# Kernel tuning notes

Measured on AMD Instinct MI355X. Metric: run time of the kernel, lower is better.

## Reference

```python
import jax, jax.numpy as jnp
import numpy as np

NEG_SLOPE = 0.2
LN_EPS = 1e-5
NUM_LAYERS = 4
H = 3            # num heads (both modalities)
C_MOL = 512      # molecule channels (in == out, required by the cat in forward)
C_PROT = 1280    # protein channels
VOCAB = 512 * 9 + 1
G_MOL = 512      # molecule graphs
G_PROT = 32      # protein graphs


def _with_self_loops(src, dst, n):
    loop = jnp.arange(n, dtype=src.dtype)
    return jnp.concatenate([src, loop]), jnp.concatenate([dst, loop])


def gat_conv(x, src, dst, W, a_src, a_dst, bias):
    """PyG GATConv, concat=False (head-mean), add_self_loops=True.
    x: [N, Fin], W: [Fin, H*C], a_src/a_dst: [H, C], bias: [C]."""
    n = x.shape[0]
    h = (x @ W).reshape(n, a_src.shape[0], a_src.shape[1])   # [N,H,C]
    al_s = jnp.sum(h * a_src, axis=-1)                       # [N,H]
    al_d = jnp.sum(h * a_dst, axis=-1)                       # [N,H]
    s, d = _with_self_loops(src, dst, n)
    e = jax.nn.leaky_relu(al_s[s] + al_d[d], NEG_SLOPE)      # [E+N,H]
    m = jax.ops.segment_max(e, d, num_segments=n)            # segment softmax (stable)
    m = jnp.where(jnp.isfinite(m), m, 0.0)
    p = jnp.exp(e - m[d])
    z = jax.ops.segment_sum(p, d, num_segments=n)
    alpha = p / (z[d] + 1e-16)                               # [E+N,H]
    out = jax.ops.segment_sum(h[s] * alpha[:, :, None], d, num_segments=n)  # [N,H,C]
    return out.mean(axis=1) + bias                           # concat=False -> head mean


def layer_norm(x, g, b):
    mu = x.mean(-1, keepdims=True)
    var = ((x - mu) ** 2).mean(-1, keepdims=True)
    return (x - mu) * jax.lax.rsqrt(var + LN_EPS) * g + b


def mean_pool(x, batch, num_graphs):
    s = jax.ops.segment_sum(x, batch, num_segments=num_graphs)
    cnt = jax.ops.segment_sum(jnp.ones((x.shape[0],), x.dtype), batch, num_segments=num_graphs)
    return s / jnp.maximum(cnt, 1.0)[:, None]


def setup_inputs() -> dict:
    key = jax.random.key(0)
    ks = jax.random.split(key, 20)
    n_mol, e_mol = 40000, 80000
    n_prot, e_prot = 8000, 64000
    drug_x = jax.random.randint(ks[0], (n_mol, 9), 0, VOCAB)
    mol_edge_index = jax.random.randint(ks[1], (2, e_mol), 0, n_mol)
    mol_batch = jnp.sort(jax.random.randint(ks[2], (n_mol,), 0, G_MOL))
    prot_x = jax.random.normal(ks[3], (n_prot, C_PROT), jnp.float32)
    prot_edge_index = jax.random.randint(ks[4], (2, e_prot), 0, n_prot)
    prot_batch = jnp.sort(jax.random.randint(ks[5], (n_prot,), 0, G_PROT))
    sc = 0.02
    emb = (jax.random.normal(ks[6], (VOCAB, C_MOL), jnp.float32) * sc).at[0].set(0.0)  # padding_idx=0
    mol_W = jax.random.normal(ks[7], (NUM_LAYERS, C_MOL, H * C_MOL), jnp.float32) * sc
    mol_asrc = jax.random.normal(ks[8], (NUM_LAYERS, H, C_MOL), jnp.float32) * sc
    mol_adst = jax.random.normal(ks[9], (NUM_LAYERS, H, C_MOL), jnp.float32) * sc
    mol_bias = jnp.zeros((NUM_LAYERS, C_MOL), jnp.float32)
    mol_ln_g = jnp.ones((NUM_LAYERS, C_MOL), jnp.float32)
    mol_ln_b = jnp.zeros((NUM_LAYERS, C_MOL), jnp.float32)
    prot_W = jax.random.normal(ks[10], (NUM_LAYERS, C_PROT, H * C_PROT), jnp.float32) * sc
    prot_asrc = jax.random.normal(ks[11], (NUM_LAYERS, H, C_PROT), jnp.float32) * sc
    prot_adst = jax.random.normal(ks[12], (NUM_LAYERS, H, C_PROT), jnp.float32) * sc
    prot_bias = jnp.zeros((NUM_LAYERS, C_PROT), jnp.float32)
    prot_ln_g = jnp.ones((NUM_LAYERS, C_PROT), jnp.float32)
    prot_ln_b = jnp.zeros((NUM_LAYERS, C_PROT), jnp.float32)
    return dict(drug_x=drug_x, mol_edge_index=mol_edge_index, mol_batch=mol_batch,
                prot_x=prot_x, prot_edge_index=prot_edge_index, prot_batch=prot_batch,
                emb=emb, mol_W=mol_W, mol_asrc=mol_asrc, mol_adst=mol_adst,
                mol_bias=mol_bias, mol_ln_g=mol_ln_g, mol_ln_b=mol_ln_b,
                prot_W=prot_W, prot_asrc=prot_asrc, prot_adst=prot_adst,
                prot_bias=prot_bias, prot_ln_g=prot_ln_g, prot_ln_b=prot_ln_b)


def reference(drug_x, mol_edge_index, mol_batch, prot_x, prot_edge_index, prot_batch,
              emb, mol_W, mol_asrc, mol_adst, mol_bias, mol_ln_g, mol_ln_b,
              prot_W, prot_asrc, prot_adst, prot_bias, prot_ln_g, prot_ln_b):
    # dropout layers are identity (eval mode)
    mol_x = emb[drug_x].mean(axis=-2)                       # [N_mol, C_MOL]
    mol_feats = [mean_pool(mol_x, mol_batch, G_MOL)]
    prot_feats = [mean_pool(prot_x, prot_batch, G_PROT)]
    msrc, mdst = mol_edge_index[0], mol_edge_index[1]
    psrc, pdst = prot_edge_index[0], prot_edge_index[1]
    px = prot_x
    for i in range(NUM_LAYERS):
        mol_x = gat_conv(mol_x, msrc, mdst, mol_W[i], mol_asrc[i], mol_adst[i], mol_bias[i])
        mol_x = layer_norm(mol_x, mol_ln_g[i], mol_ln_b[i])
        px = gat_conv(px, psrc, pdst, prot_W[i], prot_asrc[i], prot_adst[i], prot_bias[i])
        px = layer_norm(px, prot_ln_g[i], prot_ln_b[i])
        mol_feats.append(mean_pool(mol_x, mol_batch, G_MOL))
        prot_feats.append(mean_pool(px, prot_batch, G_PROT))
    return jnp.stack(mol_feats, axis=1), jnp.stack(prot_feats, axis=1)  # [G,5,C] each
```

## Files before the change

### kernel.cpp

```cpp
#include <hip/hip_runtime.h>
#include <cstdint>


constexpr int H_HEADS = 3;
constexpr float NEG_SLOPE = 0.2f;
constexpr float LN_EPS = 1e-5f;
constexpr int N_MOL = 40000, E_MOL = 80000, C_MOL = 512, G_MOL = 512;
constexpr int N_PROT = 8000, E_PROT = 64000, C_PROT = 1280, G_PROT = 32;
constexpr int LAYERS = 4;
constexpr int MPAD_MOL = 40064;
constexpr int MPAD_PROT = 8064;

typedef unsigned short u16;
typedef __attribute__((ext_vector_type(8))) short short8v;
typedef __attribute__((ext_vector_type(4))) unsigned short ushort4v;
typedef __attribute__((ext_vector_type(4))) float f32x4;

__device__ __forceinline__ float bf2f(u16 s) {
    union { unsigned u; float f; } v; v.u = ((unsigned)s) << 16; return v.f;
}
__device__ __forceinline__ u16 f2bf(float f) {
    union { float f; unsigned u; } v; v.f = f;
    return (u16)((v.u + 0x7fffu + ((v.u >> 16) & 1u)) >> 16);
}

__device__ __forceinline__ void g2l16(const void* g, void* l) {
    __builtin_amdgcn_global_load_lds((const __attribute__((address_space(1))) void*)g,
                                     (__attribute__((address_space(3))) void*)l, 16, 0, 0);
}


__global__ void set_int_kernel(int* p, int v, int n) {
    int i = blockIdx.x * blockDim.x + threadIdx.x;
    if (i < n) p[i] = v;
}

__global__ void zero_f32_kernel(float* p, int n) {
    int i = blockIdx.x * blockDim.x + threadIdx.x;
    if (i < n) p[i] = 0.f;
}

__global__ void copy_int_kernel(const int* __restrict__ s, int* __restrict__ d, int n) {
    int i = blockIdx.x * blockDim.x + threadIdx.x;
    if (i < n) d[i] = s[i];
}

__global__ void hist_kernel(const int* __restrict__ keys, int n, int* __restrict__ cnt) {
    int i = blockIdx.x * blockDim.x + threadIdx.x;
    if (i < n) atomicAdd(&cnt[keys[i]], 1);
}

__global__ void scan_kernel(const int* __restrict__ in, int* __restrict__ out, int n) {
    __shared__ int sums[1024];
    const int t = threadIdx.x;
    const int chunk = (n + 1023) / 1024;
    const int start = t * chunk;
    const int end = min(start + chunk, n);
    int s = 0;
    for (int i = start; i < end; ++i) s += in[i];
    sums[t] = s;
    __syncthreads();
    if (t == 0) {
        int acc = 0;
        for (int i = 0; i < 1024; ++i) { int v = sums[i]; sums[i] = acc; acc += v; }
        out[n] = acc;
    }
    __syncthreads();
    int acc = sums[t];
    for (int i = start; i < end; ++i) { out[i] = acc; acc += in[i]; }
}

__global__ void fill_self_kernel(int* __restrict__ pos, int* __restrict__ srcl, int n) {
    int i = blockIdx.x * blockDim.x + threadIdx.x;
    if (i < n) { int slot = atomicAdd(&pos[i], 1); srcl[slot] = i; }
}

__global__ void fill_edge_kernel(const int* __restrict__ src, const int* __restrict__ dst, int e,
                                 int* __restrict__ pos, int* __restrict__ srcl) {
    int i = blockIdx.x * blockDim.x + threadIdx.x;
    if (i < e) { int slot = atomicAdd(&pos[dst[i]], 1); srcl[slot] = src[i]; }
}

__global__ void f32_to_bf16(const float* __restrict__ in, u16* __restrict__ out, int n) {
    int i = blockIdx.x * blockDim.x + threadIdx.x;
    if (i < n) out[i] = f2bf(in[i]);
}


__global__ void embed_mean_kernel(const int* __restrict__ drug_x, const float* __restrict__ emb,
                                  u16* __restrict__ out) {
    const int n = blockIdx.x;
    __shared__ int idx[9];
    if (threadIdx.x < 9) idx[threadIdx.x] = drug_x[n * 9 + threadIdx.x];
    __syncthreads();
    const int c = threadIdx.x;
    float s = 0.f;
#pragma unroll
    for (int t = 0; t < 9; ++t) s += emb[(size_t)idx[t] * C_MOL + c];
    out[(size_t)n * C_MOL + c] = f2bf(s * (1.f / 9.f));
}


template <int CIN, int COUT>
__global__ __launch_bounds__(256) void fold_attn(const float* __restrict__ W,
                                                 const float* __restrict__ asrc,
                                                 const float* __restrict__ adst,
                                                 float* __restrict__ wsrc, float* __restrict__ wdst) {
    const int i = blockIdx.x;
    const int tid = threadIdx.x;
    __shared__ float rb[8];
    const float* Wr = W + (size_t)i * (H_HEADS * COUT);
    for (int h = 0; h < H_HEADS; ++h) {
        float ss = 0.f, sd = 0.f;
        for (int c = tid; c < COUT; c += 256) {
            const float w = Wr[h * COUT + c];
            ss += w * asrc[h * COUT + c];
            sd += w * adst[h * COUT + c];
        }
        for (int o = 32; o; o >>= 1) { ss += __shfl_down(ss, o); sd += __shfl_down(sd, o); }
        if ((tid & 63) == 0) { rb[tid >> 6] = ss; rb[4 + (tid >> 6)] = sd; }
        __syncthreads();
        if (tid == 0) {
            wsrc[h * CIN + i] = rb[0] + rb[1] + rb[2] + rb[3];
            wdst[h * CIN + i] = rb[4] + rb[5] + rb[6] + rb[7];
        }
        __syncthreads();
    }
}


__global__ __launch_bounds__(256) void transposeW(const float* __restrict__ W, u16* __restrict__ Wt,
                                                  int COUT, size_t headStride, int ldn) {
    __shared__ float t[32][33];
    const int h = blockIdx.z;
    const int n0 = blockIdx.x * 32, k0 = blockIdx.y * 32;
    const int tx = threadIdx.x & 31, ty = threadIdx.x >> 5;
#pragma unroll
    for (int q = 0; q < 4; ++q)
        t[ty + q * 8][tx] = W[(size_t)(k0 + ty + q * 8) * (H_HEADS * COUT) + h * COUT + n0 + tx];
    __syncthreads();
#pragma unroll
    for (int q = 0; q < 4; ++q)
        Wt[(size_t)h * headStride + (size_t)(n0 + ty + q * 8) * ldn + k0 + tx] =
            f2bf(t[tx][ty + q * 8]);
}


template <int C>
__global__ void attn_logits(const u16* __restrict__ x, const float* __restrict__ wsrc,
                            const float* __restrict__ wdst, float* __restrict__ als,
                            float* __restrict__ ald) {
    constexpr int PER = C / 64;
    const int n = blockIdx.x, lane = threadIdx.x;
    const u16* xr = x + (size_t)n * C + lane * PER;
    float xv[PER];
#pragma unroll
    for (int i = 0; i < PER; i += 4) {
        const ushort4v v = *(const ushort4v*)(xr + i);
        xv[i] = bf2f(v.x); xv[i + 1] = bf2f(v.y); xv[i + 2] = bf2f(v.z); xv[i + 3] = bf2f(v.w);
    }
    for (int h = 0; h < H_HEADS; ++h) {
        const float* ws = wsrc + h * C + lane * PER;
        const float* wd = wdst + h * C + lane * PER;
        float ss = 0.f, sd = 0.f;
#pragma unroll
        for (int i = 0; i < PER; i += 4) {
            const float4 a = *(const float4*)(ws + i);
            const float4 b = *(const float4*)(wd + i);
            ss += xv[i] * a.x + xv[i + 1] * a.y + xv[i + 2] * a.z + xv[i + 3] * a.w;
            sd += xv[i] * b.x + xv[i + 1] * b.y + xv[i + 2] * b.z + xv[i + 3] * b.w;
        }
        for (int o = 32; o; o >>= 1) { ss += __shfl_down(ss, o); sd += __shfl_down(sd, o); }
        if (lane == 0) { als[n * H_HEADS + h] = ss; ald[n * H_HEADS + h] = sd; }
    }
}


__global__ void alpha_kernel(const float* __restrict__ als, const float* __restrict__ ald,
                             const int* __restrict__ indptr, const int* __restrict__ srcl,
                             float* __restrict__ alphaw) {
    const int n = blockIdx.x, lane = threadIdx.x;
    if (lane >= H_HEADS) return;
    const int beg = indptr[n], end = indptr[n + 1];
    const float ad = ald[n * H_HEADS + lane];
    float m = -1e30f;
    for (int e = beg; e < end; ++e) {
        float v = als[srcl[e] * H_HEADS + lane] + ad;
        v = v >= 0.f ? v : NEG_SLOPE * v;
        m = fmaxf(m, v);
    }
    float z = 0.f;
    for (int e = beg; e < end; ++e) {
        float v = als[srcl[e] * H_HEADS + lane] + ad;
        v = v >= 0.f ? v : NEG_SLOPE * v;
        z += __expf(v - m);
    }
    const float zi = 1.f / (z + 1e-16f);
    for (int e = beg; e < end; ++e) {
        float v = als[srcl[e] * H_HEADS + lane] + ad;
        v = v >= 0.f ? v : NEG_SLOPE * v;
        alphaw[e * H_HEADS + lane] = __expf(v - m) * zi;
    }
}


template <int C>
__global__ void aggregate_head(const u16* __restrict__ x, const float* __restrict__ alphaw,
                               const int* __restrict__ indptr, const int* __restrict__ srcl,
                               int head, u16* __restrict__ aggH) {
    const int n = blockIdx.x, tid = threadIdx.x;
    const int beg = indptr[n], end = indptr[n + 1];
    float a0 = 0.f, a1 = 0.f, a2 = 0.f, a3 = 0.f;
    for (int e = beg; e < end; ++e) {
        const float a = alphaw[e * H_HEADS + head];
        const ushort4v v = *(const ushort4v*)(x + (size_t)srcl[e] * C + tid * 4);
        a0 += a * bf2f(v.x); a1 += a * bf2f(v.y); a2 += a * bf2f(v.z); a3 += a * bf2f(v.w);
    }
    ushort4v r;
    r.x = f2bf(a0); r.y = f2bf(a1); r.z = f2bf(a2); r.w = f2bf(a3);
    *(ushort4v*)(aggH + (size_t)n * C + tid * 4) = r;
}


template <int C>
__global__ void aggregate_all3(const u16* __restrict__ x, const float* __restrict__ alphaw,
                               const int* __restrict__ indptr, const int* __restrict__ srcl,
                               u16* __restrict__ aggAll) {
    const int n = blockIdx.x, tid = threadIdx.x;
    const int beg = indptr[n], end = indptr[n + 1];
    float acc[H_HEADS][4];
#pragma unroll
    for (int h = 0; h < H_HEADS; ++h)
#pragma unroll
        for (int j = 0; j < 4; ++j) acc[h][j] = 0.f;
    for (int e = beg; e < end; ++e) {
        const float a0 = alphaw[e * H_HEADS + 0];
        const float a1 = alphaw[e * H_HEADS + 1];
        const float a2 = alphaw[e * H_HEADS + 2];
        const ushort4v v = *(const ushort4v*)(x + (size_t)srcl[e] * C + tid * 4);
        const float f0 = bf2f(v.x), f1 = bf2f(v.y), f2 = bf2f(v.z), f3 = bf2f(v.w);
        acc[0][0] += a0 * f0; acc[0][1] += a0 * f1; acc[0][2] += a0 * f2; acc[0][3] += a0 * f3;
        acc[1][0] += a1 * f0; acc[1][1] += a1 * f1; acc[1][2] += a1 * f2; acc[1][3] += a1 * f3;
        acc[2][0] += a2 * f0; acc[2][1] += a2 * f1; acc[2][2] += a2 * f2; acc[2][3] += a2 * f3;
    }
    u16* o = aggAll + (size_t)n * (3 * C) + tid * 4;
#pragma unroll
    for (int h = 0; h < H_HEADS; ++h) {
        ushort4v r;
        r.x = f2bf(acc[h][0]); r.y = f2bf(acc[h][1]); r.z = f2bf(acc[h][2]); r.w = f2bf(acc[h][3]);
        *(ushort4v*)(o + h * C) = r;
    }
}


template <int BETA>
__global__ __launch_bounds__(256) void gemm_mfma(const u16* __restrict__ A,
                                                 const u16* __restrict__ Bt,
                                                 u16* __restrict__ C, int M, int N, int K) {
    __shared__ u16 As[64][40];
    __shared__ u16 Bs[256][40];
    const int tid = threadIdx.x;
    const int w = tid >> 6;
    const int l = tid & 63;
    const int bm = blockIdx.y * 64;
    const int bn = blockIdx.x * 256;
    const f32x4 zf = {0.f, 0.f, 0.f, 0.f};
    f32x4 acc[4][4];
#pragma unroll
    for (int i = 0; i < 4; ++i)
#pragma unroll
        for (int j = 0; j < 4; ++j) acc[i][j] = zf;

    const int arow = tid >> 2, aseg = tid & 3;
    const u16* Ab = A + (size_t)(bm + arow) * K + aseg * 8;
    for (int k0 = 0; k0 < K; k0 += 32) {
        const float4 av = *(const float4*)(Ab + k0);
        float4 bv[4];
#pragma unroll
        for (int q = 0; q < 4; ++q) {
            const int c = q * 256 + tid;
            bv[q] = *(const float4*)(Bt + (size_t)(bn + (c >> 2)) * K + k0 + (c & 3) * 8);
        }
        __syncthreads();
        *(float4*)&As[arow][aseg * 8] = av;
#pragma unroll
        for (int q = 0; q < 4; ++q) {
            const int c = q * 256 + tid;
            *(float4*)&Bs[c >> 2][(c & 3) * 8] = bv[q];
        }
        __syncthreads();
        const int koff = 8 * (l >> 4);
        const int rl = l & 15;
        short8v af[4], bfr[4];
#pragma unroll
        for (int fm = 0; fm < 4; ++fm) af[fm] = *(const short8v*)&As[fm * 16 + rl][koff];
#pragma unroll
        for (int fn = 0; fn < 4; ++fn) bfr[fn] = *(const short8v*)&Bs[w * 64 + fn * 16 + rl][koff];
#pragma unroll
        for (int fm = 0; fm < 4; ++fm)
#pragma unroll
            for (int fn = 0; fn < 4; ++fn)
                acc[fm][fn] =
                    __builtin_amdgcn_mfma_f32_16x16x32_bf16(af[fm], bfr[fn], acc[fm][fn], 0, 0, 0);
    }
    const int r0 = (l >> 4) * 4;
    const int cn = l & 15;
#pragma unroll
    for (int fm = 0; fm < 4; ++fm)
#pragma unroll
        for (int fn = 0; fn < 4; ++fn) {
            u16* Cp = C + (size_t)(bm + fm * 16 + r0) * N + bn + w * 64 + fn * 16 + cn;
#pragma unroll
            for (int r = 0; r < 4; ++r) {
                float v = acc[fm][fn][r];
                if (BETA) v += bf2f(Cp[(size_t)r * N]);
                Cp[(size_t)r * N] = f2bf(v);
            }
        }
}


__global__ __launch_bounds__(256) void gemm_mfma128(const u16* __restrict__ A,
                                                    const u16* __restrict__ Bt,
                                                    u16* __restrict__ Cout,
                                                    int M, int N, int K) {
    __shared__ u16 lds[17408];
    const int tid = threadIdx.x;
    const int w = tid >> 6, l = tid & 63;
    const int wr = w >> 1, wc = w & 1;
    const size_t bm = (size_t)blockIdx.y * 128, bn = (size_t)blockIdx.x * 128;
    const f32x4 zf = {0.f, 0.f, 0.f, 0.f};
    f32x4 acc[4][4];
#pragma unroll
    for (int i = 0; i < 4; ++i)
#pragma unroll
        for (int j = 0; j < 4; ++j) acc[i][j] = zf;

    const int srow = w * 32 + (l >> 3);
    const int sseg = (l & 7) ^ (l >> 3);
    const u16* Ab = A + (bm + srow) * (size_t)K + sseg * 8;
    const u16* Bb = Bt + (bn + srow) * (size_t)K + sseg * 8;

    for (int k0 = 0; k0 < K; k0 += 64) {
#pragma unroll
        for (int q = 0; q < 4; ++q)
            g2l16(Ab + k0 + (size_t)q * 8 * K, lds + (w * 4 + q) * 512);
#pragma unroll
        for (int q = 0; q < 4; ++q)
            g2l16(Bb + k0 + (size_t)q * 8 * K, lds + 8192 + (w * 4 + q) * 512);
        __syncthreads();
#pragma unroll
        for (int kk = 0; kk < 2; ++kk) {
            short8v af[4], bfr[4];
#pragma unroll
            for (int fm = 0; fm < 4; ++fm) {
                const int row = wr * 64 + fm * 16 + (l & 15);
                const int seg = (kk * 4 + (l >> 4)) ^ (row & 7);
                af[fm] = *(const short8v*)&lds[row * 64 + seg * 8];
            }
#pragma unroll
            for (int fn = 0; fn < 4; ++fn) {
                const int row = wc * 64 + fn * 16 + (l & 15);
                const int seg = (kk * 4 + (l >> 4)) ^ (row & 7);
                bfr[fn] = *(const short8v*)&lds[8192 + row * 64 + seg * 8];
            }
#pragma unroll
            for (int fm = 0; fm < 4; ++fm)
#pragma unroll
                for (int fn = 0; fn < 4; ++fn)
                    acc[fm][fn] = __builtin_amdgcn_mfma_f32_16x16x32_bf16(af[fm], bfr[fn],
                                                                          acc[fm][fn], 0, 0, 0);
        }
        __syncthreads();
    }

#pragma unroll
    for (int fm = 0; fm < 4; ++fm) {
        const int row = wr * 64 + fm * 16 + (l >> 4) * 4;
#pragma unroll
        for (int fn = 0; fn < 4; ++fn) {
            const int col = wc * 64 + fn * 16 + (l & 15);
#pragma unroll
            for (int r = 0; r < 4; ++r) lds[(row + r) * 136 + col] = f2bf(acc[fm][fn][r]);
        }
    }
    __syncthreads();
    const int orow = tid >> 1, ohalf = tid & 1;
    u16* Crow = Cout + (bm + orow) * (size_t)N + bn + ohalf * 64;
    const u16* Lrow = lds + orow * 136 + ohalf * 64;
#pragma unroll
    for (int i = 0; i < 8; ++i)
        *(float4*)(Crow + i * 8) = *(const float4*)(Lrow + i * 8);
}


template <int C>
__global__ __launch_bounds__(256) void ln_kernel(const u16* __restrict__ acc,
                                                 const float* __restrict__ bias,
                                                 const float* __restrict__ g,
                                                 const float* __restrict__ b,
                                                 u16* __restrict__ xout) {
    constexpr int PER = C / 256;
    const int n = blockIdx.x, tid = threadIdx.x;
    const u16* ar = acc + (size_t)n * C;
    float vals[PER];
    float s1 = 0.f, s2 = 0.f;
    constexpr float invH = 1.f / (float)H_HEADS;
#pragma unroll
    for (int i = 0; i < PER; ++i) {
        const int c = i * 256 + tid;
        const float v = bf2f(ar[c]) * invH + bias[c];
        vals[i] = v;
        s1 += v;
        s2 += v * v;
    }
    __shared__ float red[2][4];
    for (int o = 32; o; o >>= 1) { s1 += __shfl_down(s1, o); s2 += __shfl_down(s2, o); }
    if ((tid & 63) == 0) { red[0][tid >> 6] = s1; red[1][tid >> 6] = s2; }
    __syncthreads();
    const float t1 = red[0][0] + red[0][1] + red[0][2] + red[0][3];
    const float t2 = red[1][0] + red[1][1] + red[1][2] + red[1][3];
    const float mu = t1 / C;
    const float var = t2 / C - mu * mu;
    const float rstd = rsqrtf(var + LN_EPS);
    u16* xr = xout + (size_t)n * C;
#pragma unroll
    for (int i = 0; i < PER; ++i) {
        const int c = i * 256 + tid;
        xr[c] = f2bf((vals[i] - mu) * rstd * g[c] + b[c]);
    }
}


template <int C, int S>
__global__ void pool_atomic(const u16* __restrict__ x, const int* __restrict__ goff,
                            float* __restrict__ out, int layer) {
    const int g = blockIdx.x, seg = blockIdx.y;
    const int beg = goff[g], end = goff[g + 1];
    const int len = end - beg;
    const int s0 = beg + (len * seg) / S;
    const int s1 = beg + (len * (seg + 1)) / S;
    if (s0 >= s1) return;
    const float inv = 1.f / fmaxf((float)len, 1.f);
    const int tid = threadIdx.x;
    float a0 = 0.f, a1 = 0.f, a2 = 0.f, a3 = 0.f;
    for (int n = s0; n < s1; ++n) {
        const ushort4v v = *(const ushort4v*)(x + (size_t)n * C + tid * 4);
        a0 += bf2f(v.x); a1 += bf2f(v.y); a2 += bf2f(v.z); a3 += bf2f(v.w);
    }
    float* o = out + ((size_t)g * (LAYERS + 1) + layer) * C + tid * 4;
    atomicAdd(o + 0, a0 * inv);
    atomicAdd(o + 1, a1 * inv);
    atomicAdd(o + 2, a2 * inv);
    atomicAdd(o + 3, a3 * inv);
}


extern "C" void kernel_launch(void* const* d_in, const int* in_sizes, int n_in, void* d_out,
                              int out_size, void* d_ws, size_t ws_size, hipStream_t stream) {
    const int* drug_x      = (const int*)d_in[0];
    const int* mol_ei      = (const int*)d_in[1];
    const int* mol_batch   = (const int*)d_in[2];
    const float* prot_in   = (const float*)d_in[3];
    const int* prot_ei     = (const int*)d_in[4];
    const int* prot_batch  = (const int*)d_in[5];
    const float* emb       = (const float*)d_in[6];
    const float* mol_W     = (const float*)d_in[7];
    const float* mol_asrc  = (const float*)d_in[8];
    const float* mol_adst  = (const float*)d_in[9];
    const float* mol_bias  = (const float*)d_in[10];
    const float* mol_lng   = (const float*)d_in[11];
    const float* mol_lnb   = (const float*)d_in[12];
    const float* prot_W    = (const float*)d_in[13];
    const float* prot_asrc = (const float*)d_in[14];
    const float* prot_adst = (const float*)d_in[15];
    const float* prot_bias = (const float*)d_in[16];
    const float* prot_lng  = (const float*)d_in[17];
    const float* prot_lnb  = (const float*)d_in[18];

    if (ws_size < (size_t)157000000) return;
    const bool BIG = ws_size >= (size_t)240500000;

    char* base = (char*)d_ws;
    size_t off = 0;
    auto alloc = [&](size_t bytes) -> void* {
        void* r = base + off;
        off = (off + bytes + 255) & ~(size_t)255;
        return r;
    };
    u16* x_mol  = (u16*)alloc((size_t)N_MOL * C_MOL * 2);
    u16* x_prot = (u16*)alloc((size_t)N_PROT * C_PROT * 2);
    u16* Wt     = (u16*)alloc((size_t)H_HEADS * C_PROT * C_PROT * 2);
    float* wsrc = (float*)alloc((size_t)H_HEADS * C_PROT * 4);
    float* wdst = (float*)alloc((size_t)H_HEADS * C_PROT * 4);
    float* als  = (float*)alloc((size_t)N_MOL * H_HEADS * 4);
    float* ald  = (float*)alloc((size_t)N_MOL * H_HEADS * 4);
    float* alphaw = (float*)alloc((size_t)(E_MOL + N_MOL) * H_HEADS * 4);
    int* mol_indptr  = (int*)alloc((N_MOL + 1) * 4);
    int* mol_pos     = (int*)alloc(N_MOL * 4);
    int* mol_srcl    = (int*)alloc((E_MOL + N_MOL) * 4);
    int* prot_indptr = (int*)alloc((N_PROT + 1) * 4);
    int* prot_pos    = (int*)alloc(N_PROT * 4);
    int* prot_srcl   = (int*)alloc((E_PROT + N_PROT) * 4);
    int* cnt         = (int*)alloc(N_MOL * 4);
    int* mol_goff    = (int*)alloc((G_MOL + 1) * 4);
    int* prot_goff   = (int*)alloc((G_PROT + 1) * 4);
    int* gcnt        = (int*)alloc(G_MOL * 4);
    u16 *aggAll = nullptr, *aggH = nullptr, *outb = nullptr;
    if (BIG) {
        aggAll = (u16*)alloc((size_t)3 * MPAD_MOL * C_MOL * 2);
        outb   = (u16*)alloc((size_t)MPAD_MOL * C_MOL * 2);
    } else {
        aggH = (u16*)alloc((size_t)N_MOL * C_MOL * 2);
        outb = (u16*)alloc((size_t)N_MOL * C_MOL * 2);
    }

    float* out_mol  = (float*)d_out;
    float* out_prot = (float*)d_out + (size_t)G_MOL * (LAYERS + 1) * C_MOL;

    zero_f32_kernel<<<(out_size + 255) / 256, 256, 0, stream>>>((float*)d_out, out_size);

    set_int_kernel<<<(N_MOL + 255) / 256, 256, 0, stream>>>(cnt, 1, N_MOL);
    hist_kernel<<<(E_MOL + 255) / 256, 256, 0, stream>>>(mol_ei + E_MOL, E_MOL, cnt);
    scan_kernel<<<1, 1024, 0, stream>>>(cnt, mol_indptr, N_MOL);
    copy_int_kernel<<<(N_MOL + 255) / 256, 256, 0, stream>>>(mol_indptr, mol_pos, N_MOL);
    fill_self_kernel<<<(N_MOL + 255) / 256, 256, 0, stream>>>(mol_pos, mol_srcl, N_MOL);
    fill_edge_kernel<<<(E_MOL + 255) / 256, 256, 0, stream>>>(mol_ei, mol_ei + E_MOL, E_MOL, mol_pos,
                                                              mol_srcl);

    set_int_kernel<<<(N_PROT + 255) / 256, 256, 0, stream>>>(cnt, 1, N_PROT);
    hist_kernel<<<(E_PROT + 255) / 256, 256, 0, stream>>>(prot_ei + E_PROT, E_PROT, cnt);
    scan_kernel<<<1, 1024, 0, stream>>>(cnt, prot_indptr, N_PROT);
    copy_int_kernel<<<(N_PROT + 255) / 256, 256, 0, stream>>>(prot_indptr, prot_pos, N_PROT);
    fill_self_kernel<<<(N_PROT + 255) / 256, 256, 0, stream>>>(prot_pos, prot_srcl, N_PROT);
    fill_edge_kernel<<<(E_PROT + 255) / 256, 256, 0, stream>>>(prot_ei, prot_ei + E_PROT, E_PROT,
                                                               prot_pos, prot_srcl);

    set_int_kernel<<<(G_MOL + 255) / 256, 256, 0, stream>>>(gcnt, 0, G_MOL);
    hist_kernel<<<(N_MOL + 255) / 256, 256, 0, stream>>>(mol_batch, N_MOL, gcnt);
    scan_kernel<<<1, 1024, 0, stream>>>(gcnt, mol_goff, G_MOL);
    set_int_kernel<<<(G_PROT + 255) / 256, 256, 0, stream>>>(gcnt, 0, G_PROT);
    hist_kernel<<<(N_PROT + 255) / 256, 256, 0, stream>>>(prot_batch, N_PROT, gcnt);
    scan_kernel<<<1, 1024, 0, stream>>>(gcnt, prot_goff, G_PROT);

    f32_to_bf16<<<(N_PROT * C_PROT + 255) / 256, 256, 0, stream>>>(prot_in, x_prot, N_PROT * C_PROT);
    embed_mean_kernel<<<N_MOL, C_MOL, 0, stream>>>(drug_x, emb, x_mol);
    pool_atomic<C_MOL, 8><<<dim3(G_MOL, 8), C_MOL / 4, 0, stream>>>(x_mol, mol_goff, out_mol, 0);
    pool_atomic<C_PROT, 64><<<dim3(G_PROT, 64), C_PROT / 4, 0, stream>>>(x_prot, prot_goff, out_prot, 0);

    for (int l = 0; l < LAYERS; ++l) {
        {
            const float* Wl = mol_W + (size_t)l * C_MOL * (H_HEADS * C_MOL);
            fold_attn<C_MOL, C_MOL><<<C_MOL, 256, 0, stream>>>(
                Wl, mol_asrc + (size_t)l * H_HEADS * C_MOL, mol_adst + (size_t)l * H_HEADS * C_MOL,
                wsrc, wdst);
            attn_logits<C_MOL><<<N_MOL, 64, 0, stream>>>(x_mol, wsrc, wdst, als, ald);
            alpha_kernel<<<N_MOL, 64, 0, stream>>>(als, ald, mol_indptr, mol_srcl, alphaw);
            if (BIG) {
                transposeW<<<dim3(C_MOL / 32, C_MOL / 32, H_HEADS), 256, 0, stream>>>(
                    Wl, Wt, C_MOL, (size_t)C_MOL, 3 * C_MOL);
                aggregate_all3<C_MOL><<<N_MOL, C_MOL / 4, 0, stream>>>(x_mol, alphaw, mol_indptr,
                                                                       mol_srcl, aggAll);
                gemm_mfma128<<<dim3(C_MOL / 128, MPAD_MOL / 128), 256, 0, stream>>>(
                    aggAll, Wt, outb, MPAD_MOL, C_MOL, 3 * C_MOL);
            } else {
                transposeW<<<dim3(C_MOL / 32, C_MOL / 32, H_HEADS), 256, 0, stream>>>(
                    Wl, Wt, C_MOL, (size_t)C_MOL * C_MOL, C_MOL);
                for (int h = 0; h < H_HEADS; ++h) {
                    aggregate_head<C_MOL><<<N_MOL, C_MOL / 4, 0, stream>>>(x_mol, alphaw, mol_indptr,
                                                                           mol_srcl, h, aggH);
                    const u16* Bh = Wt + (size_t)h * C_MOL * C_MOL;
                    if (h == 0)
                        gemm_mfma<0><<<dim3(C_MOL / 256, N_MOL / 64), 256, 0, stream>>>(
                            aggH, Bh, outb, N_MOL, C_MOL, C_MOL);
                    else
                        gemm_mfma<1><<<dim3(C_MOL / 256, N_MOL / 64), 256, 0, stream>>>(
                            aggH, Bh, outb, N_MOL, C_MOL, C_MOL);
                }
            }
            ln_kernel<C_MOL><<<N_MOL, 256, 0, stream>>>(outb, mol_bias + (size_t)l * C_MOL,
                                                        mol_lng + (size_t)l * C_MOL,
                                                        mol_lnb + (size_t)l * C_MOL, x_mol);
            pool_atomic<C_MOL, 8><<<dim3(G_MOL, 8), C_MOL / 4, 0, stream>>>(x_mol, mol_goff, out_mol,
                                                                            l + 1);
        }
        {
            const float* Wl = prot_W + (size_t)l * C_PROT * (H_HEADS * C_PROT);
            fold_attn<C_PROT, C_PROT><<<C_PROT, 256, 0, stream>>>(
                Wl, prot_asrc + (size_t)l * H_HEADS * C_PROT,
                prot_adst + (size_t)l * H_HEADS * C_PROT, wsrc, wdst);
            attn_logits<C_PROT><<<N_PROT, 64, 0, stream>>>(x_prot, wsrc, wdst, als, ald);
            alpha_kernel<<<N_PROT, 64, 0, stream>>>(als, ald, prot_indptr, prot_srcl, alphaw);
            if (BIG) {
                transposeW<<<dim3(C_PROT / 32, C_PROT / 32, H_HEADS), 256, 0, stream>>>(
                    Wl, Wt, C_PROT, (size_t)C_PROT, 3 * C_PROT);
                aggregate_all3<C_PROT><<<N_PROT, C_PROT / 4, 0, stream>>>(x_prot, alphaw, prot_indptr,
                                                                          prot_srcl, aggAll);
                gemm_mfma128<<<dim3(C_PROT / 128, MPAD_PROT / 128), 256, 0, stream>>>(
                    aggAll, Wt, outb, MPAD_PROT, C_PROT, 3 * C_PROT);
            } else {
                transposeW<<<dim3(C_PROT / 32, C_PROT / 32, H_HEADS), 256, 0, stream>>>(
                    Wl, Wt, C_PROT, (size_t)C_PROT * C_PROT, C_PROT);
                for (int h = 0; h < H_HEADS; ++h) {
                    aggregate_head<C_PROT><<<N_PROT, C_PROT / 4, 0, stream>>>(
                        x_prot, alphaw, prot_indptr, prot_srcl, h, aggH);
                    const u16* Bh = Wt + (size_t)h * C_PROT * C_PROT;
                    if (h == 0)
                        gemm_mfma<0><<<dim3(C_PROT / 256, N_PROT / 64), 256, 0, stream>>>(
                            aggH, Bh, outb, N_PROT, C_PROT, C_PROT);
                    else
                        gemm_mfma<1><<<dim3(C_PROT / 256, N_PROT / 64), 256, 0, stream>>>(
                            aggH, Bh, outb, N_PROT, C_PROT, C_PROT);
                }
            }
            ln_kernel<C_PROT><<<N_PROT, 256, 0, stream>>>(outb, prot_bias + (size_t)l * C_PROT,
                                                          prot_lng + (size_t)l * C_PROT,
                                                          prot_lnb + (size_t)l * C_PROT, x_prot);
            pool_atomic<C_PROT, 64><<<dim3(G_PROT, 64), C_PROT / 4, 0, stream>>>(x_prot, prot_goff,
                                                                                 out_prot, l + 1);
        }
    }
}
```

Baseline: 2.372 ms.

## Fuse attention logits into LayerNorm, add 256-wide XCD-swizzled GEMM, wave-per-node aggregation

Several changes land together. Attention-vector folding is hoisted for all layers up front, and the next layer's per-node attention logits are computed inside the LayerNorm kernel, which removes one pass over the activations per layer. The softmax-weight kernel now uses one thread per (node, head) instead of a mostly idle 64-thread block per node. Molecule aggregation processes one node per wave with 8-wide loads. A new 128x256-tile GEMM with 512 threads and XCD-aware block remapping replaces the 128x128 GEMM, and the small-workspace fallback path is removed. The larger GEMM tile raises LDS use and register pressure, and the logit fusion adds reductions to the LayerNorm kernel.

```diff
diff --git a/kernel.cpp b/kernel.cpp
--- a/kernel.cpp
+++ b/kernel.cpp
@@ -176,49 +176,67 @@
 }
 
 
-__global__ void alpha_kernel(const float* __restrict__ als, const float* __restrict__ ald,
-                             const int* __restrict__ indptr, const int* __restrict__ srcl,
-                             float* __restrict__ alphaw) {
-    const int n = blockIdx.x, lane = threadIdx.x;
-    if (lane >= H_HEADS) return;
+__global__ void alpha_kernel2(const float* __restrict__ als, const float* __restrict__ ald,
+                              const int* __restrict__ indptr, const int* __restrict__ srcl,
+                              float* __restrict__ alphaw, int n_nodes) {
+    const int t = blockIdx.x * blockDim.x + threadIdx.x;
+    const int n = t / H_HEADS, h = t - n * H_HEADS;
+    if (n >= n_nodes) return;
     const int beg = indptr[n], end = indptr[n + 1];
-    const float ad = ald[n * H_HEADS + lane];
+    const float ad = ald[n * H_HEADS + h];
     float m = -1e30f;
     for (int e = beg; e < end; ++e) {
-        float v = als[srcl[e] * H_HEADS + lane] + ad;
+        float v = als[srcl[e] * H_HEADS + h] + ad;
         v = v >= 0.f ? v : NEG_SLOPE * v;
         m = fmaxf(m, v);
     }
     float z = 0.f;
     for (int e = beg; e < end; ++e) {
-        float v = als[srcl[e] * H_HEADS + lane] + ad;
+        float v = als[srcl[e] * H_HEADS + h] + ad;
         v = v >= 0.f ? v : NEG_SLOPE * v;
         z += __expf(v - m);
     }
     const float zi = 1.f / (z + 1e-16f);
     for (int e = beg; e < end; ++e) {
-        float v = als[srcl[e] * H_HEADS + lane] + ad;
+        float v = als[srcl[e] * H_HEADS + h] + ad;
         v = v >= 0.f ? v : NEG_SLOPE * v;
-        alphaw[e * H_HEADS + lane] = __expf(v - m) * zi;
-    }
-}
-
-
-template <int C>
-__global__ void aggregate_head(const u16* __restrict__ x, const float* __restrict__ alphaw,
-                               const int* __restrict__ indptr, const int* __restrict__ srcl,
-                               int head, u16* __restrict__ aggH) {
-    const int n = blockIdx.x, tid = threadIdx.x;
+        alphaw[e * H_HEADS + h] = __expf(v - m) * zi;
+    }
+}
+
+
+__global__ __launch_bounds__(256) void aggregate_mol(const u16* __restrict__ x,
+                                                     const float* __restrict__ alphaw,
+                                                     const int* __restrict__ indptr,
+                                                     const int* __restrict__ srcl,
+                                                     u16* __restrict__ aggAll) {
+    const int wv = threadIdx.x >> 6, lane = threadIdx.x & 63;
+    const int n = blockIdx.x * 4 + wv;
     const int beg = indptr[n], end = indptr[n + 1];
-    float a0 = 0.f, a1 = 0.f, a2 = 0.f, a3 = 0.f;
+    float acc[H_HEADS][8];
+#pragma unroll
+    for (int h = 0; h < H_HEADS; ++h)
+#pragma unroll
+        for (int j = 0; j < 8; ++j) acc[h][j] = 0.f;
     for (int e = beg; e < end; ++e) {
-        const float a = alphaw[e * H_HEADS + head];
-        const ushort4v v = *(const ushort4v*)(x + (size_t)srcl[e] * C + tid * 4);
-        a0 += a * bf2f(v.x); a1 += a * bf2f(v.y); a2 += a * bf2f(v.z); a3 += a * bf2f(v.w);
-    }
-    ushort4v r;
-    r.x = f2bf(a0); r.y = f2bf(a1); r.z = f2bf(a2); r.w = f2bf(a3);
-    *(ushort4v*)(aggH + (size_t)n * C + tid * 4) = r;
+        const float a0 = alphaw[e * H_HEADS + 0];
+        const float a1 = alphaw[e * H_HEADS + 1];
+        const float a2 = alphaw[e * H_HEADS + 2];
+        const short8v row = *(const short8v*)(x + (size_t)srcl[e] * C_MOL + lane * 8);
+#pragma unroll
+        for (int j = 0; j < 8; ++j) {
+            const float f = bf2f((u16)row[j]);
+            acc[0][j] += a0 * f; acc[1][j] += a1 * f; acc[2][j] += a2 * f;
+        }
+    }
+    u16* o = aggAll + (size_t)n * (3 * C_MOL) + lane * 8;
+#pragma unroll
+    for (int h = 0; h < H_HEADS; ++h) {
+        short8v r;
+#pragma unroll
+        for (int j = 0; j < 8; ++j) r[j] = (short)f2bf(acc[h][j]);
+        *(short8v*)(o + h * C_MOL) = r;
+    }
 }
 
 
@@ -253,17 +271,21 @@
 }
 
 
-template <int BETA>
-__global__ __launch_bounds__(256) void gemm_mfma(const u16* __restrict__ A,
-                                                 const u16* __restrict__ Bt,
-                                                 u16* __restrict__ C, int M, int N, int K) {
-    __shared__ u16 As[64][40];
-    __shared__ u16 Bs[256][40];
+__global__ __launch_bounds__(512) void gemm_mfma256(const u16* __restrict__ A,
+                                                    const u16* __restrict__ Bt,
+                                                    u16* __restrict__ Cout,
+                                                    int N, int K, int nxch) {
+    __shared__ u16 lds[24576];
     const int tid = threadIdx.x;
-    const int w = tid >> 6;
-    const int l = tid & 63;
-    const int bm = blockIdx.y * 64;
-    const int bn = blockIdx.x * 256;
+    const int w = tid >> 6, l = tid & 63;
+    const int wr = w >> 2, wc = w & 3;
+    const int nwg = gridDim.x;
+    const int q = nwg >> 3, r = nwg & 7;
+    const int xcd = blockIdx.x & 7, idx = blockIdx.x >> 3;
+    const int wgid = (xcd < r ? xcd * (q + 1) : r * (q + 1) + (xcd - r) * q) + idx;
+    const int nx = wgid % nxch, my = wgid / nxch;
+    const size_t bm = (size_t)my * 128, bn = (size_t)nx * 256;
+
     const f32x4 zf = {0.f, 0.f, 0.f, 0.f};
     f32x4 acc[4][4];
 #pragma unroll
@@ -271,135 +293,77 @@
 #pragma unroll
         for (int j = 0; j < 4; ++j) acc[i][j] = zf;
 
-    const int arow = tid >> 2, aseg = tid & 3;
-    const u16* Ab = A + (size_t)(bm + arow) * K + aseg * 8;
-    for (int k0 = 0; k0 < K; k0 += 32) {
-        const float4 av = *(const float4*)(Ab + k0);
-        float4 bv[4];
-#pragma unroll
-        for (int q = 0; q < 4; ++q) {
-            const int c = q * 256 + tid;
-            bv[q] = *(const float4*)(Bt + (size_t)(bn + (c >> 2)) * K + k0 + (c & 3) * 8);
-        }
-        __syncthreads();
-        *(float4*)&As[arow][aseg * 8] = av;
-#pragma unroll
-        for (int q = 0; q < 4; ++q) {
-            const int c = q * 256 + tid;
-            *(float4*)&Bs[c >> 2][(c & 3) * 8] = bv[q];
-        }
-        __syncthreads();
-        const int koff = 8 * (l >> 4);
-        const int rl = l & 15;
-        short8v af[4], bfr[4];
-#pragma unroll
-        for (int fm = 0; fm < 4; ++fm) af[fm] = *(const short8v*)&As[fm * 16 + rl][koff];
-#pragma unroll
-        for (int fn = 0; fn < 4; ++fn) bfr[fn] = *(const short8v*)&Bs[w * 64 + fn * 16 + rl][koff];
-#pragma unroll
-        for (int fm = 0; fm < 4; ++fm)
-#pragma unroll
-            for (int fn = 0; fn < 4; ++fn)
-                acc[fm][fn] =
-                    __builtin_amdgcn_mfma_f32_16x16x32_bf16(af[fm], bfr[fn], acc[fm][fn], 0, 0, 0);
-    }
-    const int r0 = (l >> 4) * 4;
-    const int cn = l & 15;
-#pragma unroll
-    for (int fm = 0; fm < 4; ++fm)
-#pragma unroll
-        for (int fn = 0; fn < 4; ++fn) {
-            u16* Cp = C + (size_t)(bm + fm * 16 + r0) * N + bn + w * 64 + fn * 16 + cn;
-#pragma unroll
-            for (int r = 0; r < 4; ++r) {
-                float v = acc[fm][fn][r];
-                if (BETA) v += bf2f(Cp[(size_t)r * N]);
-                Cp[(size_t)r * N] = f2bf(v);
-            }
-        }
-}
-
-
-__global__ __launch_bounds__(256) void gemm_mfma128(const u16* __restrict__ A,
-                                                    const u16* __restrict__ Bt,
-                                                    u16* __restrict__ Cout,
-                                                    int M, int N, int K) {
-    __shared__ u16 lds[17408];
-    const int tid = threadIdx.x;
-    const int w = tid >> 6, l = tid & 63;
-    const int wr = w >> 1, wc = w & 1;
-    const size_t bm = (size_t)blockIdx.y * 128, bn = (size_t)blockIdx.x * 128;
-    const f32x4 zf = {0.f, 0.f, 0.f, 0.f};
-    f32x4 acc[4][4];
-#pragma unroll
-    for (int i = 0; i < 4; ++i)
-#pragma unroll
-        for (int j = 0; j < 4; ++j) acc[i][j] = zf;
-
-    const int srow = w * 32 + (l >> 3);
     const int sseg = (l & 7) ^ (l >> 3);
-    const u16* Ab = A + (bm + srow) * (size_t)K + sseg * 8;
-    const u16* Bb = Bt + (bn + srow) * (size_t)K + sseg * 8;
+    const u16* Ab = A + (bm + w * 16 + (l >> 3)) * (size_t)K + sseg * 8;
+    const u16* Bb = Bt + (bn + w * 32 + (l >> 3)) * (size_t)K + sseg * 8;
 
     for (int k0 = 0; k0 < K; k0 += 64) {
 #pragma unroll
-        for (int q = 0; q < 4; ++q)
-            g2l16(Ab + k0 + (size_t)q * 8 * K, lds + (w * 4 + q) * 512);
-#pragma unroll
-        for (int q = 0; q < 4; ++q)
-            g2l16(Bb + k0 + (size_t)q * 8 * K, lds + 8192 + (w * 4 + q) * 512);
+        for (int qq = 0; qq < 2; ++qq)
+            g2l16(Ab + k0 + (size_t)qq * 8 * K, lds + (w * 2 + qq) * 512);
+#pragma unroll
+        for (int qq = 0; qq < 4; ++qq)
+            g2l16(Bb + k0 + (size_t)qq * 8 * K, lds + 8192 + (w * 4 + qq) * 512);
         __syncthreads();
 #pragma unroll
         for (int kk = 0; kk < 2; ++kk) {
-            short8v af[4], bfr[4];
+            const int gs = kk * 4 + (l >> 4);
+            const int sg = (gs ^ (l & 7)) * 8;
+            short8v af[4], bf8[4];
 #pragma unroll
             for (int fm = 0; fm < 4; ++fm) {
                 const int row = wr * 64 + fm * 16 + (l & 15);
-                const int seg = (kk * 4 + (l >> 4)) ^ (row & 7);
-                af[fm] = *(const short8v*)&lds[row * 64 + seg * 8];
+                af[fm] = *(const short8v*)&lds[row * 64 + sg];
             }
 #pragma unroll
             for (int fn = 0; fn < 4; ++fn) {
                 const int row = wc * 64 + fn * 16 + (l & 15);
-                const int seg = (kk * 4 + (l >> 4)) ^ (row & 7);
-                bfr[fn] = *(const short8v*)&lds[8192 + row * 64 + seg * 8];
+                bf8[fn] = *(const short8v*)&lds[8192 + row * 64 + sg];
             }
 #pragma unroll
             for (int fm = 0; fm < 4; ++fm)
 #pragma unroll
                 for (int fn = 0; fn < 4; ++fn)
-                    acc[fm][fn] = __builtin_amdgcn_mfma_f32_16x16x32_bf16(af[fm], bfr[fn],
+                    acc[fm][fn] = __builtin_amdgcn_mfma_f32_16x16x32_bf16(af[fm], bf8[fn],
                                                                           acc[fm][fn], 0, 0, 0);
         }
         __syncthreads();
     }
 
 #pragma unroll
-    for (int fm = 0; fm < 4; ++fm) {
-        const int row = wr * 64 + fm * 16 + (l >> 4) * 4;
-#pragma unroll
-        for (int fn = 0; fn < 4; ++fn) {
-            const int col = wc * 64 + fn * 16 + (l & 15);
-#pragma unroll
-            for (int r = 0; r < 4; ++r) lds[(row + r) * 136 + col] = f2bf(acc[fm][fn][r]);
-        }
-    }
-    __syncthreads();
-    const int orow = tid >> 1, ohalf = tid & 1;
-    u16* Crow = Cout + (bm + orow) * (size_t)N + bn + ohalf * 64;
-    const u16* Lrow = lds + orow * 136 + ohalf * 64;
-#pragma unroll
-    for (int i = 0; i < 8; ++i)
-        *(float4*)(Crow + i * 8) = *(const float4*)(Lrow + i * 8);
-}
-
-
-template <int C>
+    for (int half = 0; half < 2; ++half) {
+        if (wr == half) {
+#pragma unroll
+            for (int fm = 0; fm < 4; ++fm)
+#pragma unroll
+                for (int fn = 0; fn < 4; ++fn) {
+                    const int col = wc * 64 + fn * 16 + (l & 15);
+#pragma unroll
+                    for (int rr = 0; rr < 4; ++rr)
+                        lds[(fm * 16 + (l >> 4) * 4 + rr) * 264 + col] = f2bf(acc[fm][fn][rr]);
+                }
+        }
+        __syncthreads();
+        const int lrow = tid >> 3, lseg = tid & 7;
+        u16* Crow = Cout + (bm + half * 64 + lrow) * (size_t)N + bn + lseg * 32;
+        const u16* Lr = lds + lrow * 264 + lseg * 32;
+#pragma unroll
+        for (int ii = 0; ii < 4; ++ii)
+            *(float4*)(Crow + ii * 8) = *(const float4*)(Lr + ii * 8);
+        __syncthreads();
+    }
+}
+
+
+template <int C, int LOGITS>
 __global__ __launch_bounds__(256) void ln_kernel(const u16* __restrict__ acc,
                                                  const float* __restrict__ bias,
                                                  const float* __restrict__ g,
                                                  const float* __restrict__ b,
-                                                 u16* __restrict__ xout) {
+                                                 u16* __restrict__ xout,
+                                                 const float* __restrict__ wsrc_n,
+                                                 const float* __restrict__ wdst_n,
+                                                 float* __restrict__ als, float* __restrict__ ald) {
     constexpr int PER = C / 256;
     const int n = blockIdx.x, tid = threadIdx.x;
     const u16* ar = acc + (size_t)n * C;
@@ -415,6 +379,7 @@
         s2 += v * v;
     }
     __shared__ float red[2][4];
+    __shared__ float red2[4][6];
     for (int o = 32; o; o >>= 1) { s1 += __shfl_down(s1, o); s2 += __shfl_down(s2, o); }
     if ((tid & 63) == 0) { red[0][tid >> 6] = s1; red[1][tid >> 6] = s2; }
     __syncthreads();
@@ -424,10 +389,38 @@
     const float var = t2 / C - mu * mu;
     const float rstd = rsqrtf(var + LN_EPS);
     u16* xr = xout + (size_t)n * C;
+    float ps0 = 0.f, ps1 = 0.f, ps2 = 0.f, pd0 = 0.f, pd1 = 0.f, pd2 = 0.f;
 #pragma unroll
     for (int i = 0; i < PER; ++i) {
         const int c = i * 256 + tid;
-        xr[c] = f2bf((vals[i] - mu) * rstd * g[c] + b[c]);
+        const u16 xq16 = f2bf((vals[i] - mu) * rstd * g[c] + b[c]);
+        xr[c] = xq16;
+        if (LOGITS) {
+            const float xq = bf2f(xq16);
+            ps0 += xq * wsrc_n[0 * C + c]; pd0 += xq * wdst_n[0 * C + c];
+            ps1 += xq * wsrc_n[1 * C + c]; pd1 += xq * wdst_n[1 * C + c];
+            ps2 += xq * wsrc_n[2 * C + c]; pd2 += xq * wdst_n[2 * C + c];
+        }
+    }
+    if (LOGITS) {
+        for (int o = 32; o; o >>= 1) {
+            ps0 += __shfl_down(ps0, o); ps1 += __shfl_down(ps1, o); ps2 += __shfl_down(ps2, o);
+            pd0 += __shfl_down(pd0, o); pd1 += __shfl_down(pd1, o); pd2 += __shfl_down(pd2, o);
+        }
+        __syncthreads();
+        if ((tid & 63) == 0) {
+            const int wv = tid >> 6;
+            red2[wv][0] = ps0; red2[wv][1] = ps1; red2[wv][2] = ps2;
+            red2[wv][3] = pd0; red2[wv][4] = pd1; red2[wv][5] = pd2;
+        }
+        __syncthreads();
+        if (tid == 0) {
+#pragma unroll
+            for (int h = 0; h < H_HEADS; ++h) {
+                als[n * H_HEADS + h] = red2[0][h] + red2[1][h] + red2[2][h] + red2[3][h];
+                ald[n * H_HEADS + h] = red2[0][3 + h] + red2[1][3 + h] + red2[2][3 + h] + red2[3][3 + h];
+            }
+        }
     }
 }
 
@@ -478,8 +471,7 @@
     const float* prot_lng  = (const float*)d_in[17];
     const float* prot_lnb  = (const float*)d_in[18];
 
-    if (ws_size < (size_t)157000000) return;
-    const bool BIG = ws_size >= (size_t)240500000;
+    if (ws_size < (size_t)240500000) return;
 
     char* base = (char*)d_ws;
     size_t off = 0;
@@ -490,11 +482,17 @@
     };
     u16* x_mol  = (u16*)alloc((size_t)N_MOL * C_MOL * 2);
     u16* x_prot = (u16*)alloc((size_t)N_PROT * C_PROT * 2);
+    u16* aggAll = (u16*)alloc((size_t)3 * MPAD_MOL * C_MOL * 2);
+    u16* outb   = (u16*)alloc((size_t)MPAD_MOL * C_MOL * 2);
     u16* Wt     = (u16*)alloc((size_t)H_HEADS * C_PROT * C_PROT * 2);
-    float* wsrc = (float*)alloc((size_t)H_HEADS * C_PROT * 4);
-    float* wdst = (float*)alloc((size_t)H_HEADS * C_PROT * 4);
-    float* als  = (float*)alloc((size_t)N_MOL * H_HEADS * 4);
-    float* ald  = (float*)alloc((size_t)N_MOL * H_HEADS * 4);
+    float* wsrcM = (float*)alloc((size_t)LAYERS * H_HEADS * C_MOL * 4);
+    float* wdstM = (float*)alloc((size_t)LAYERS * H_HEADS * C_MOL * 4);
+    float* wsrcP = (float*)alloc((size_t)LAYERS * H_HEADS * C_PROT * 4);
+    float* wdstP = (float*)alloc((size_t)LAYERS * H_HEADS * C_PROT * 4);
+    float* alsM = (float*)alloc((size_t)N_MOL * H_HEADS * 4);
+    float* aldM = (float*)alloc((size_t)N_MOL * H_HEADS * 4);
+    float* alsP = (float*)alloc((size_t)N_PROT * H_HEADS * 4);
+    float* aldP = (float*)alloc((size_t)N_PROT * H_HEADS * 4);
     float* alphaw = (float*)alloc((size_t)(E_MOL + N_MOL) * H_HEADS * 4);
     int* mol_indptr  = (int*)alloc((N_MOL + 1) * 4);
     int* mol_pos     = (int*)alloc(N_MOL * 4);
@@ -506,14 +504,6 @@
     int* mol_goff    = (int*)alloc((G_MOL + 1) * 4);
     int* prot_goff   = (int*)alloc((G_PROT + 1) * 4);
     int* gcnt        = (int*)alloc(G_MOL * 4);
-    u16 *aggAll = nullptr, *aggH = nullptr, *outb = nullptr;
-    if (BIG) {
-        aggAll = (u16*)alloc((size_t)3 * MPAD_MOL * C_MOL * 2);
-        outb   = (u16*)alloc((size_t)MPAD_MOL * C_MOL * 2);
-    } else {
-        aggH = (u16*)alloc((size_t)N_MOL * C_MOL * 2);
-        outb = (u16*)alloc((size_t)N_MOL * C_MOL * 2);
-    }
 
     float* out_mol  = (float*)d_out;
     float* out_prot = (float*)d_out + (size_t)G_MOL * (LAYERS + 1) * C_MOL;
@@ -543,79 +533,68 @@
     hist_kernel<<<(N_PROT + 255) / 256, 256, 0, stream>>>(prot_batch, N_PROT, gcnt);
     scan_kernel<<<1, 1024, 0, stream>>>(gcnt, prot_goff, G_PROT);
 
+    for (int l = 0; l < LAYERS; ++l) {
+        fold_attn<C_MOL, C_MOL><<<C_MOL, 256, 0, stream>>>(
+            mol_W + (size_t)l * C_MOL * (H_HEADS * C_MOL),
+            mol_asrc + (size_t)l * H_HEADS * C_MOL, mol_adst + (size_t)l * H_HEADS * C_MOL,
+            wsrcM + (size_t)l * H_HEADS * C_MOL, wdstM + (size_t)l * H_HEADS * C_MOL);
+        fold_attn<C_PROT, C_PROT><<<C_PROT, 256, 0, stream>>>(
+            prot_W + (size_t)l * C_PROT * (H_HEADS * C_PROT),
+            prot_asrc + (size_t)l * H_HEADS * C_PROT, prot_adst + (size_t)l * H_HEADS * C_PROT,
+            wsrcP + (size_t)l * H_HEADS * C_PROT, wdstP + (size_t)l * H_HEADS * C_PROT);
+    }
+
     f32_to_bf16<<<(N_PROT * C_PROT + 255) / 256, 256, 0, stream>>>(prot_in, x_prot, N_PROT * C_PROT);
     embed_mean_kernel<<<N_MOL, C_MOL, 0, stream>>>(drug_x, emb, x_mol);
     pool_atomic<C_MOL, 8><<<dim3(G_MOL, 8), C_MOL / 4, 0, stream>>>(x_mol, mol_goff, out_mol, 0);
     pool_atomic<C_PROT, 64><<<dim3(G_PROT, 64), C_PROT / 4, 0, stream>>>(x_prot, prot_goff, out_prot, 0);
+    attn_logits<C_MOL><<<N_MOL, 64, 0, stream>>>(x_mol, wsrcM, wdstM, alsM, aldM);
+    attn_logits<C_PROT><<<N_PROT, 64, 0, stream>>>(x_prot, wsrcP, wdstP, alsP, aldP);
 
     for (int l = 0; l < LAYERS; ++l) {
+        const int last = (l == LAYERS - 1);
         {
             const float* Wl = mol_W + (size_t)l * C_MOL * (H_HEADS * C_MOL);
-            fold_attn<C_MOL, C_MOL><<<C_MOL, 256, 0, stream>>>(
-                Wl, mol_asrc + (size_t)l * H_HEADS * C_MOL, mol_adst + (size_t)l * H_HEADS * C_MOL,
-                wsrc, wdst);
-            attn_logits<C_MOL><<<N_MOL, 64, 0, stream>>>(x_mol, wsrc, wdst, als, ald);
-            alpha_kernel<<<N_MOL, 64, 0, stream>>>(als, ald, mol_indptr, mol_srcl, alphaw);
-            if (BIG) {
-                transposeW<<<dim3(C_MOL / 32, C_MOL / 32, H_HEADS), 256, 0, stream>>>(
-                    Wl, Wt, C_MOL, (size_t)C_MOL, 3 * C_MOL);
-                aggregate_all3<C_MOL><<<N_MOL, C_MOL / 4, 0, stream>>>(x_mol, alphaw, mol_indptr,
-                                                                       mol_srcl, aggAll);
-                gemm_mfma128<<<dim3(C_MOL / 128, MPAD_MOL / 128), 256, 0, stream>>>(
-                    aggAll, Wt, outb, MPAD_MOL, C_MOL, 3 * C_MOL);
-            } else {
-                transposeW<<<dim3(C_MOL / 32, C_MOL / 32, H_HEADS), 256, 0, stream>>>(
-                    Wl, Wt, C_MOL, (size_t)C_MOL * C_MOL, C_MOL);
-                for (int h = 0; h < H_HEADS; ++h) {
-                    aggregate_head<C_MOL><<<N_MOL, C_MOL / 4, 0, stream>>>(x_mol, alphaw, mol_indptr,
-                                                                           mol_srcl, h, aggH);
-                    const u16* Bh = Wt + (size_t)h * C_MOL * C_MOL;
-                    if (h == 0)
-                        gemm_mfma<0><<<dim3(C_MOL / 256, N_MOL / 64), 256, 0, stream>>>(
-                            aggH, Bh, outb, N_MOL, C_MOL, C_MOL);
-                    else
-                        gemm_mfma<1><<<dim3(C_MOL / 256, N_MOL / 64), 256, 0, stream>>>(
-                            aggH, Bh, outb, N_MOL, C_MOL, C_MOL);
-                }
-            }
-            ln_kernel<C_MOL><<<N_MOL, 256, 0, stream>>>(outb, mol_bias + (size_t)l * C_MOL,
-                                                        mol_lng + (size_t)l * C_MOL,
-                                                        mol_lnb + (size_t)l * C_MOL, x_mol);
+            alpha_kernel2<<<(N_MOL * H_HEADS + 255) / 256, 256, 0, stream>>>(
+                alsM, aldM, mol_indptr, mol_srcl, alphaw, N_MOL);
+            transposeW<<<dim3(C_MOL / 32, C_MOL / 32, H_HEADS), 256, 0, stream>>>(
+                Wl, Wt, C_MOL, (size_t)C_MOL, 3 * C_MOL);
+            aggregate_mol<<<N_MOL / 4, 256, 0, stream>>>(x_mol, alphaw, mol_indptr, mol_srcl, aggAll);
+            gemm_mfma256<<<(C_MOL / 256) * (MPAD_MOL / 128), 512, 0, stream>>>(
+                aggAll, Wt, outb, C_MOL, 3 * C_MOL, C_MOL / 256);
+            if (last)
+                ln_kernel<C_MOL, 0><<<N_MOL, 256, 0, stream>>>(
+                    outb, mol_bias + (size_t)l * C_MOL, mol_lng + (size_t)l * C_MOL,
+                    mol_lnb + (size_t)l * C_MOL, x_mol, nullptr, nullptr, nullptr, nullptr);
+            else
+                ln_kernel<C_MOL, 1><<<N_MOL, 256, 0, stream>>>(
+                    outb, mol_bias + (size_t)l * C_MOL, mol_lng + (size_t)l * C_MOL,
+                    mol_lnb + (size_t)l * C_MOL, x_mol,
+                    wsrcM + (size_t)(l + 1) * H_HEADS * C_MOL,
+                    wdstM + (size_t)(l + 1) * H_HEADS * C_MOL, alsM, aldM);
             pool_atomic<C_MOL, 8><<<dim3(G_MOL, 8), C_MOL / 4, 0, stream>>>(x_mol, mol_goff, out_mol,
                                                                             l + 1);
         }
         {
             const float* Wl = prot_W + (size_t)l * C_PROT * (H_HEADS * C_PROT);
-            fold_attn<C_PROT, C_PROT><<<C_PROT, 256, 0, stream>>>(
-                Wl, prot_asrc + (size_t)l * H_HEADS * C_PROT,
-                prot_adst + (size_t)l * H_HEADS * C_PROT, wsrc, wdst);
-            attn_logits<C_PROT><<<N_PROT, 64, 0, stream>>>(x_prot, wsrc, wdst, als, ald);
-            alpha_kernel<<<N_PROT, 64, 0, stream>>>(als, ald, prot_indptr, prot_srcl, alphaw);
-            if (BIG) {
-                transposeW<<<dim3(C_PROT / 32, C_PROT / 32, H_HEADS), 256, 0, stream>>>(
-                    Wl, Wt, C_PROT, (size_t)C_PROT, 3 * C_PROT);
-                aggregate_all3<C_PROT><<<N_PROT, C_PROT / 4, 0, stream>>>(x_prot, alphaw, prot_indptr,
-                                                                          prot_srcl, aggAll);
-                gemm_mfma128<<<dim3(C_PROT / 128, MPAD_PROT / 128), 256, 0, stream>>>(
-                    aggAll, Wt, outb, MPAD_PROT, C_PROT, 3 * C_PROT);
-            } else {
-                transposeW<<<dim3(C_PROT / 32, C_PROT / 32, H_HEADS), 256, 0, stream>>>(
-                    Wl, Wt, C_PROT, (size_t)C_PROT * C_PROT, C_PROT);
-                for (int h = 0; h < H_HEADS; ++h) {
-                    aggregate_head<C_PROT><<<N_PROT, C_PROT / 4, 0, stream>>>(
-                        x_prot, alphaw, prot_indptr, prot_srcl, h, aggH);
-                    const u16* Bh = Wt + (size_t)h * C_PROT * C_PROT;
-                    if (h == 0)
-                        gemm_mfma<0><<<dim3(C_PROT / 256, N_PROT / 64), 256, 0, stream>>>(
-                            aggH, Bh, outb, N_PROT, C_PROT, C_PROT);
-                    else
-                        gemm_mfma<1><<<dim3(C_PROT / 256, N_PROT / 64), 256, 0, stream>>>(
-                            aggH, Bh, outb, N_PROT, C_PROT, C_PROT);
-                }
-            }
-            ln_kernel<C_PROT><<<N_PROT, 256, 0, stream>>>(outb, prot_bias + (size_t)l * C_PROT,
-                                                          prot_lng + (size_t)l * C_PROT,
-                                                          prot_lnb + (size_t)l * C_PROT, x_prot);
+            alpha_kernel2<<<(N_PROT * H_HEADS + 255) / 256, 256, 0, stream>>>(
+                alsP, aldP, prot_indptr, prot_srcl, alphaw, N_PROT);
+            transposeW<<<dim3(C_PROT / 32, C_PROT / 32, H_HEADS), 256, 0, stream>>>(
+                Wl, Wt, C_PROT, (size_t)C_PROT, 3 * C_PROT);
+            aggregate_all3<C_PROT><<<N_PROT, C_PROT / 4, 0, stream>>>(x_prot, alphaw, prot_indptr,
+                                                                      prot_srcl, aggAll);
+            gemm_mfma256<<<(C_PROT / 256) * (MPAD_PROT / 128), 512, 0, stream>>>(
+                aggAll, Wt, outb, C_PROT, 3 * C_PROT, C_PROT / 256);
+            if (last)
+                ln_kernel<C_PROT, 0><<<N_PROT, 256, 0, stream>>>(
+                    outb, prot_bias + (size_t)l * C_PROT, prot_lng + (size_t)l * C_PROT,
+                    prot_lnb + (size_t)l * C_PROT, x_prot, nullptr, nullptr, nullptr, nullptr);
+            else
+                ln_kernel<C_PROT, 1><<<N_PROT, 256, 0, stream>>>(
+                    outb, prot_bias + (size_t)l * C_PROT, prot_lng + (size_t)l * C_PROT,
+                    prot_lnb + (size_t)l * C_PROT, x_prot,
+                    wsrcP + (size_t)(l + 1) * H_HEADS * C_PROT,
+                    wdstP + (size_t)(l + 1) * H_HEADS * C_PROT, alsP, aldP);
             pool_atomic<C_PROT, 64><<<dim3(G_PROT, 64), C_PROT / 4, 0, stream>>>(x_prot, prot_goff,
                                                                                  out_prot, l + 1);
         }
```

After: 2.439 ms. +2.8%, slower.
